# Optimization experiments

Hardware: AMD Instinct MI355X
Metric: run time of the kernel (lower is better)

## Reference

```python
import jax, jax.numpy as jnp
import numpy as np

B, S, DDENSE, D, V, F, K = 8192, 26, 13, 32, 100000, 8, 7


def setup_inputs() -> dict:
    key = jax.random.key(0)
    ks = jax.random.split(key, 24)
    n = lambda i, shape, s=0.05: (jax.random.normal(ks[i], shape, dtype=jnp.float32) * s)
    return {
        'sparse_inputs': jax.random.randint(ks[0], (B, S), 0, V),
        'dense_inputs': jax.random.normal(ks[1], (B, DDENSE), dtype=jnp.float32),
        'gen_table': n(2, (V, D), 0.1), 'gen_W': n(3, (DDENSE, D)), 'gen_b': jnp.zeros((D,), jnp.float32),
        'cls_table': n(4, (V, D), 0.1), 'cls_W': n(5, (DDENSE, D)), 'cls_b': jnp.zeros((D,), jnp.float32),
        'conv_k0': n(6, (K, 1, 1, F)), 'conv_b0': jnp.zeros((F,), jnp.float32),
        'fc_W0': n(7, (13 * D * F, 3 * D)), 'fc_b0': jnp.zeros((3 * D,), jnp.float32),
        'conv_k1': n(8, (K, 1, F, F)), 'conv_b1': jnp.zeros((F,), jnp.float32),
        'fc_W1': n(9, (6 * D * F, 3 * D)), 'fc_b1': jnp.zeros((3 * D,), jnp.float32),
        'mlp_W1': n(10, (1584, 128)), 'mlp_b1': jnp.zeros((128,), jnp.float32),
        'bn_gamma': jnp.ones((128,), jnp.float32), 'bn_beta': jnp.zeros((128,), jnp.float32),
        'bn_mean': jnp.zeros((128,), jnp.float32), 'bn_var': jnp.ones((128,), jnp.float32),
        'out_W': n(11, (128, 1)), 'out_b': jnp.zeros((1,), jnp.float32),
    }


def _embed(sparse_inputs, dense_inputs, table, W, b):
    sp = table[sparse_inputs]                       # [B, 26, 32]
    dn = (dense_inputs @ W + b)[:, None, :]         # [B, 1, 32]
    return jnp.concatenate([sp, dn], axis=1)        # [B, 27, 32]


def _conv_tanh(x, k, b):
    y = jax.lax.conv_general_dilated(x, k, (1, 1), 'SAME',
                                     dimension_numbers=('NHWC', 'HWIO', 'NHWC'))
    return jnp.tanh(y + b)


def _maxpool2(x):  # MaxPooling2D((2,1), padding='valid') on NHWC
    return jax.lax.reduce_window(x, -jnp.inf, jax.lax.max,
                                 (1, 2, 1, 1), (1, 2, 1, 1), 'VALID')


def _forward(sparse_inputs, dense_inputs, gen_table, gen_W, gen_b,
             cls_table, cls_W, cls_b, conv_k0, conv_b0, fc_W0, fc_b0,
             conv_k1, conv_b1, fc_W1, fc_b1, mlp_W1, mlp_b1,
             bn_gamma, bn_beta, bn_mean, bn_var, out_W, out_b):
    embs_gen = _embed(sparse_inputs, dense_inputs, gen_table, gen_W, gen_b)
    embs_cls = _embed(sparse_inputs, dense_inputs, cls_table, cls_W, cls_b)

    x = embs_gen[..., None]                         # [B, 27, 32, 1] NHWC
    new_feats = []
    for ck, cb, fw, fb in ((conv_k0, conv_b0, fc_W0, fc_b0),
                           (conv_k1, conv_b1, fc_W1, fc_b1)):
        x = _maxpool2(_conv_tanh(x, ck, cb))
        flat = x.reshape(x.shape[0], -1)
        new_feats.append(jnp.tanh(flat @ fw + fb))  # [B, 96]

    gen = jnp.concatenate(new_feats, axis=1).reshape(x.shape[0], -1, D)  # [B, 6, 32]
    aug = jnp.concatenate([embs_cls, gen], axis=1)                       # [B, 33, 32]

    # pairwise inner products = upper triangle of Gram matrix, combinations order
    gram = jnp.einsum('bnd,bmd->bnm', aug, aug)
    iu, ju = jnp.triu_indices(aug.shape[1], k=1)
    ip = gram[:, iu, ju]                            # [B, 528]

    h = jnp.concatenate([ip, aug.reshape(aug.shape[0], -1)], axis=1)     # [B, 1584]
    h = jax.nn.relu(h @ mlp_W1 + mlp_b1)
    h = (h - bn_mean) * jax.lax.rsqrt(bn_var + 1e-3) * bn_gamma + bn_beta
    return jax.nn.sigmoid(h @ out_W + out_b)        # [B, 1]


def reference(sparse_inputs, dense_inputs, gen_table, gen_W, gen_b,
              cls_table, cls_W, cls_b, conv_k0, conv_b0, fc_W0, fc_b0,
              conv_k1, conv_b1, fc_W1, fc_b1, mlp_W1, mlp_b1,
              bn_gamma, bn_beta, bn_mean, bn_var, out_W, out_b):
    return _forward(sparse_inputs, dense_inputs, gen_table, gen_W, gen_b,
                    cls_table, cls_W, cls_b, conv_k0, conv_b0, fc_W0, fc_b0,
                    conv_k1, conv_b1, fc_W1, fc_b1, mlp_W1, mlp_b1,
                    bn_gamma, bn_beta, bn_mean, bn_var, out_W, out_b)
```

## Files before the change

### kernel.cpp

```cpp
#include <hip/hip_runtime.h>
#include <hip/hip_bf16.h>
#include <math.h>

#define BATCH 8192

typedef unsigned short bf16_t;
typedef _Float16 f16_t;
typedef __attribute__((ext_vector_type(2))) _Float16 h2_t;
typedef __attribute__((ext_vector_type(8))) short short8;
typedef __attribute__((ext_vector_type(4))) float f32x4;

union U32H2 { unsigned int u; h2_t h; };

__device__ __forceinline__ float bf2f(bf16_t u) {
    union { unsigned int i; float f; } v; v.i = ((unsigned int)u) << 16; return v.f;
}
__device__ __forceinline__ bf16_t f2bf(float f) {
    union { float f; unsigned int i; } v; v.f = f;
    unsigned int x = v.i;
    unsigned int r = (x + 0x7FFFu + ((x >> 16) & 1u)) >> 16;
    return (bf16_t)r;
}
__device__ __forceinline__ float fast_tanh(float x) {
    float ax = fabsf(x);
    float e = __expf(ax + ax);
    float t = 1.0f - 2.0f * __builtin_amdgcn_rcpf(e + 1.0f);
    return copysignf(t, x);
}


__device__ __forceinline__ void wpack_one(
    const float* __restrict__ src, bf16_t* __restrict__ dst,
    int P, int N, int NT, int Ksrc)
{
    int e = P & 7, lane = (P >> 3) & 63, idx = P >> 9;
    int nt = idx % NT, git = idx / NT;
    int n = nt * 16 + (lane & 15);
    int k = git * 32 + (lane >> 4) * 8 + e;
    dst[P] = (k < Ksrc) ? f2bf(src[(size_t)k * N + n]) : (bf16_t)0;
}

__global__ __launch_bounds__(256) void k_wpack(
    const float* __restrict__ W0, const float* __restrict__ W1, const float* __restrict__ W2,
    bf16_t* __restrict__ Wt0, bf16_t* __restrict__ Wt1, bf16_t* __restrict__ Wt2)
{
    const int m = blockIdx.y;
    const int P = blockIdx.x * 256 + threadIdx.x;
    if (m == 0)      { if (P < 319488) wpack_one(W0, Wt0, P, 96, 6, 3328); }
    else if (m == 1) { if (P < 147456) wpack_one(W1, Wt1, P, 96, 6, 1536); }
    else             { if (P < 204800) wpack_one(W2, Wt2, P, 128, 8, 1584); }
}

__global__ __launch_bounds__(256) void k_conv_fused(
    const int* __restrict__ sp, const float* __restrict__ dn,
    const float* __restrict__ gen_table, const float* __restrict__ gen_W, const float* __restrict__ gen_b,
    const float* __restrict__ k0, const float* __restrict__ b0,
    const float* __restrict__ k1, const float* __restrict__ b1,
    bf16_t* __restrict__ pooled0, bf16_t* __restrict__ pooled1)
{
    __shared__ float embGt[2][32][28];
    __shared__ unsigned int x0[2 * 13 * 32 * 4];
    __shared__ float k0s[56], k1s[448], b0s[8], b1s[8];
    __shared__ int ids[52];
    __shared__ float dloc[26];
    const int t = threadIdx.x;
    const int half = t >> 7, tt = t & 127;
    const int b = blockIdx.x * 2 + half;

    if (tt < 26) ids[half * 26 + tt] = sp[b * 26 + tt];
    if (tt >= 32 && tt < 45) dloc[half * 13 + tt - 32] = dn[b * 13 + (tt - 32)];
    if (t < 56) k0s[t] = k0[t];
    if (t >= 64 && t < 72) b0s[t - 64] = b0[t - 64];
    if (t >= 72 && t < 80) b1s[t - 72] = b1[t - 72];
    for (int i = t; i < 448; i += 256) k1s[i] = k1[i];
    __syncthreads();

    for (int i = tt; i < 416; i += 128) {
        int s_ = i >> 4, d = (i & 15) * 2;
        float2 v = *(const float2*)(gen_table + (size_t)ids[half * 26 + s_] * 32 + d);
        embGt[half][d][s_] = v.x;
        embGt[half][d + 1][s_] = v.y;
    }
    if (tt < 32) {
        float a = gen_b[tt];
        #pragma unroll
        for (int k = 0; k < 13; k++) a += dloc[half * 13 + k] * gen_W[k * 32 + tt];
        embGt[half][tt][26] = a;
    }
    __syncthreads();

    bf16_t* p0base = pooled0 + ((size_t)(b >> 4) * 416) * 128 + (b & 15) * 8;

    {
        const int w = tt >> 2, f0 = (tt & 3) * 2;
        const float* xp = &embGt[half][w][0];
        float xr[28];
        #pragma unroll
        for (int q = 0; q < 7; q++) {
            float4 v = *(const float4*)(xp + 4 * q);
            xr[4 * q] = v.x; xr[4 * q + 1] = v.y; xr[4 * q + 2] = v.z; xr[4 * q + 3] = v.w;
        }
        float k0r[7][2];
        #pragma unroll
        for (int tap = 0; tap < 7; tap++) {
            k0r[tap][0] = k0s[tap * 8 + f0];
            k0r[tap][1] = k0s[tap * 8 + f0 + 1];
        }
        const float b00 = b0s[f0], b01 = b0s[f0 + 1];
        #pragma unroll
        for (int hp = 0; hp < 13; hp++) {
            float p00 = b00, p01 = b01, p10 = b00, p11 = b01;
            #pragma unroll
            for (int tap = 0; tap < 7; tap++) {
                const int h0 = 2 * hp + tap - 3;
                if (h0 >= 0 && h0 < 27) {
                    p00 += xr[h0] * k0r[tap][0];
                    p01 += xr[h0] * k0r[tap][1];
                }
                const int h1 = 2 * hp + 1 + tap - 3;
                if (h1 >= 0 && h1 < 27) {
                    p10 += xr[h1] * k0r[tap][0];
                    p11 += xr[h1] * k0r[tap][1];
                }
            }
            float m0 = fast_tanh(fmaxf(p00, p10));
            float m1 = fast_tanh(fmaxf(p01, p11));
            unsigned int pk = (unsigned int)f2bf(m0) | ((unsigned int)f2bf(m1) << 16);
            *(unsigned int*)(p0base + (hp * 32 + w) * 128 + f0) = pk;
            U32H2 hx; hx.h = h2_t{(f16_t)m0, (f16_t)m1};
            x0[half * 1664 + hp * 128 + w * 4 + (tt & 3)] = hx.u;
        }
    }
    __syncthreads();

    {
        const int w1 = t >> 3, fo = t & 7;
        h2_t kh[7][4];
        #pragma unroll
        for (int tap = 0; tap < 7; tap++)
            #pragma unroll
            for (int q = 0; q < 4; q++)
                kh[tap][q] = h2_t{(f16_t)k1s[tap * 64 + (2 * q) * 8 + fo],
                                  (f16_t)k1s[tap * 64 + (2 * q + 1) * 8 + fo]};
        const f16_t bbh = (f16_t)b1s[fo];

        #pragma unroll
        for (int s = 0; s < 2; s++) {
            h2_t acc[12];
            #pragma unroll
            for (int r = 0; r < 12; r++) acc[r] = h2_t{bbh, (f16_t)0.f};
            #pragma unroll
            for (int hh = 0; hh < 13; hh++) {
                uint4 v = *(const uint4*)&x0[s * 1664 + hh * 128 + w1 * 4];
                U32H2 c0, c1, c2, c3;
                c0.u = v.x; c1.u = v.y; c2.u = v.z; c3.u = v.w;
                h2_t x2[4] = { c0.h, c1.h, c2.h, c3.h };
                #pragma unroll
                for (int tap = 0; tap < 7; tap++) {
                    const int r = hh + 3 - tap;
                    if (r >= 0 && r < 12) {
                        #pragma unroll
                        for (int q = 0; q < 4; q++) acc[r] += x2[q] * kh[tap][q];
                    }
                }
            }
            const int bs = blockIdx.x * 2 + s;
            bf16_t* p1base = pooled1 + ((size_t)(bs >> 4) * 192) * 128 + (bs & 15) * 8;
            #pragma unroll
            for (int hp = 0; hp < 6; hp++) {
                float a0 = (float)acc[2 * hp][0] + (float)acc[2 * hp][1];
                float a1 = (float)acc[2 * hp + 1][0] + (float)acc[2 * hp + 1][1];
                float m = fast_tanh(fmaxf(a0, a1));
                p1base[(hp * 32 + w1) * 128 + fo] = f2bf(m);
            }
        }
    }
}

__global__ __launch_bounds__(256) void k_fc_mfma(
    const bf16_t* __restrict__ A0, const bf16_t* __restrict__ Wt0, float* __restrict__ P0,
    const bf16_t* __restrict__ A1, const bf16_t* __restrict__ Wt1, float* __restrict__ P1)
{
    const int which = blockIdx.z;
    const bf16_t* A  = which ? A1 : A0;
    const bf16_t* Wt = which ? Wt1 : Wt0;
    float* P = (which ? P1 : P0) + (size_t)blockIdx.y * (BATCH * 96);
    const int K = which ? 1536 : 3328;
    const int iters = which ? 12 : 26;

    const int t = threadIdx.x, w = t >> 6, l = t & 63;
    const int lane15 = l & 15, quad = l >> 4;
    const int rb = blockIdx.x * 4 + w;
    const int kb = blockIdx.y * (K >> 2);

    const bf16_t* ap = A + ((size_t)rb * (K >> 3) + (kb >> 3) + quad) * 128 + lane15 * 8;
    const bf16_t* bp = Wt + (size_t)(kb >> 5) * 3072 + l * 8;
    f32x4 acc[6] = {};

    #pragma unroll 2
    for (int it = 0; it < iters; it++) {
        short8 a = *(const short8*)(ap + it * 512);
        #pragma unroll
        for (int nt = 0; nt < 6; nt++) {
            short8 bf = *(const short8*)(bp + it * 3072 + nt * 512);
            acc[nt] = __builtin_amdgcn_mfma_f32_16x16x32_bf16(a, bf, acc[nt], 0, 0, 0);
        }
    }
    const int baser = blockIdx.x * 64 + w * 16 + quad * 4;
    #pragma unroll
    for (int nt = 0; nt < 6; nt++)
        #pragma unroll
        for (int i = 0; i < 4; i++)
            P[(size_t)(baser + i) * 96 + nt * 16 + lane15] = acc[nt][i];
}

__global__ __launch_bounds__(256) void k_build_h(
    const int* __restrict__ sp, const float* __restrict__ dn,
    const float* __restrict__ cls_table, const float* __restrict__ cls_W, const float* __restrict__ cls_b,
    const float* __restrict__ p0, const float* __restrict__ fb0,
    const float* __restrict__ p1, const float* __restrict__ fb1,
    bf16_t* __restrict__ h)
{
    __shared__ bf16_t augs[4][33][40];
    __shared__ float grams[4][32][34];
    const int t = threadIdx.x, wv = t >> 6, l = t & 63;
    const int b = blockIdx.x * 4 + wv;
    bf16_t (*aug)[40] = augs[wv];
    float (*gram)[34] = grams[wv];

    const int myid = (l < 26) ? sp[b * 26 + l] : 0;

    for (int i = l; i < 416; i += 64) {
        int s_ = i >> 4, d = (i & 15) * 2;
        int id = __shfl(myid, s_);
        float2 v = *(const float2*)(cls_table + (size_t)id * 32 + d);
        unsigned int pk = (unsigned int)f2bf(v.x) | ((unsigned int)f2bf(v.y) << 16);
        *(unsigned int*)&aug[s_][d] = pk;
    }
    if (l < 32) {
        float a = cls_b[l];
        #pragma unroll
        for (int k = 0; k < 13; k++) a += dn[b * 13 + k] * cls_W[k * 32 + l];
        aug[26][l] = f2bf(a);
    }
    for (int i = l; i < 192; i += 64) {
        int n = 27 + (i >> 5), d = i & 31;
        float s;
        if (i < 96) {
            size_t o = (size_t)b * 96 + i;
            s = p0[o] + p0[o + 786432] + p0[o + 2 * 786432] + p0[o + 3 * 786432] + fb0[i];
        } else {
            int j = i - 96; size_t o = (size_t)b * 96 + j;
            s = p1[o] + p1[o + 786432] + p1[o + 2 * 786432] + p1[o + 3 * 786432] + fb1[j];
        }
        aug[n][d] = f2bf(fast_tanh(s));
    }

    const int m16 = l & 15, quad = l >> 4;
    short8 a0 = *(const short8*)&aug[m16][quad * 8];
    short8 a1 = *(const short8*)&aug[16 + m16][quad * 8];
    f32x4 c00 = {}, c01 = {}, c11 = {};
    c00 = __builtin_amdgcn_mfma_f32_16x16x32_bf16(a0, a0, c00, 0, 0, 0);
    c01 = __builtin_amdgcn_mfma_f32_16x16x32_bf16(a0, a1, c01, 0, 0, 0);
    c11 = __builtin_amdgcn_mfma_f32_16x16x32_bf16(a1, a1, c11, 0, 0, 0);
    #pragma unroll
    for (int i = 0; i < 4; i++) {
        gram[quad * 4 + i][m16] = c00[i];
        gram[quad * 4 + i][16 + m16] = c01[i];
        gram[16 + quad * 4 + i][16 + m16] = c11[i];
    }
    if (l < 32) {
        float s = 0.f;
        #pragma unroll
        for (int kk = 0; kk < 16; kk++) {
            unsigned int x = *(const unsigned int*)&aug[l][2 * kk];
            unsigned int y = *(const unsigned int*)&aug[32][2 * kk];
            s += bf2f((bf16_t)(x & 0xFFFFu)) * bf2f((bf16_t)(y & 0xFFFFu));
            s += bf2f((bf16_t)(x >> 16)) * bf2f((bf16_t)(y >> 16));
        }
        gram[l][32] = s;
    }

    bf16_t* hbp = h + ((size_t)(b >> 4) * 200) * 128 + (b & 15) * 8;
    for (int idx = l; idx < 528; idx += 64) {
        int k = 528 + 2 * idx;
        *(unsigned int*)(hbp + (k >> 3) * 128 + (k & 7)) = *(const unsigned int*)&aug[idx >> 4][(idx & 15) * 2];
    }
    if (l < 8) {
        int k = 1584 + 2 * l;
        *(unsigned int*)(hbp + (k >> 3) * 128 + (k & 7)) = 0u;
    }
    for (int pp = l; pp < 264; pp += 64) {
        int p = 2 * pp;
        int i = (int)((65.0f - sqrtf(4225.0f - 8.0f * (float)p)) * 0.5f);
        int st = (i * (65 - i)) >> 1;
        if (st > p) { i--; st = (i * (65 - i)) >> 1; }
        else { int st2 = ((i + 1) * (64 - i)) >> 1; if (st2 <= p) { i++; st = st2; } }
        int j = i + 1 + (p - st);
        float s0, s1;
        if (j < 32) { s0 = gram[i][j]; s1 = gram[i][j + 1]; }
        else        { s0 = gram[i][32]; s1 = gram[i + 1][i + 2]; }
        unsigned int pk = (unsigned int)f2bf(s0) | ((unsigned int)f2bf(s1) << 16);
        *(unsigned int*)(hbp + (p >> 3) * 128 + (p & 7)) = pk;
    }
}

__global__ __launch_bounds__(256) void k_mlp_mfma(
    const bf16_t* __restrict__ h, const bf16_t* __restrict__ Wt2,
    const float* __restrict__ b1, const float* __restrict__ gamma,
    const float* __restrict__ beta, const float* __restrict__ mean,
    const float* __restrict__ var, const float* __restrict__ outW,
    const float* __restrict__ outb, float* __restrict__ out)
{
    __shared__ float lds[2 * 16 * 65];
    __shared__ float red2[32];
    const int t = threadIdx.x, w = t >> 6, l = t & 63;
    const int lane15 = l & 15, quad = l >> 4;
    const int nhalf = w & 1, khalf = w >> 1;

    const bf16_t* ap = h + ((size_t)blockIdx.x * 200 + khalf * 100 + quad) * 128 + lane15 * 8;
    const bf16_t* bp = Wt2 + ((size_t)khalf * 25 * 8 + nhalf * 4) * 512 + l * 8;
    f32x4 acc[4] = {};

    #pragma unroll 2
    for (int it = 0; it < 25; it++) {
        short8 a = *(const short8*)(ap + it * 512);
        #pragma unroll
        for (int nt = 0; nt < 4; nt++) {
            short8 bf = *(const short8*)(bp + it * 4096 + nt * 512);
            acc[nt] = __builtin_amdgcn_mfma_f32_16x16x32_bf16(a, bf, acc[nt], 0, 0, 0);
        }
    }

    if (khalf == 1) {
        #pragma unroll
        for (int nt = 0; nt < 4; nt++)
            #pragma unroll
            for (int i = 0; i < 4; i++)
                lds[nhalf * 1040 + (quad * 4 + i) * 65 + nt * 16 + lane15] = acc[nt][i];
    }
    __syncthreads();
    if (khalf == 0) {
        float pl[4] = { 0.f, 0.f, 0.f, 0.f };
        #pragma unroll
        for (int nt = 0; nt < 4; nt++) {
            int c = nhalf * 64 + nt * 16 + lane15;
            float sc = gamma[c] * rsqrtf(var[c] + 1e-3f);
            float sh = beta[c] - mean[c] * sc;
            float ow = outW[c], bb = b1[c];
            #pragma unroll
            for (int i = 0; i < 4; i++) {
                float v = acc[nt][i] + lds[nhalf * 1040 + (quad * 4 + i) * 65 + nt * 16 + lane15] + bb;
                v = fmaxf(v, 0.f);
                pl[i] += (v * sc + sh) * ow;
            }
        }
        #pragma unroll
        for (int m = 1; m < 16; m <<= 1)
            #pragma unroll
            for (int i = 0; i < 4; i++) pl[i] += __shfl_xor(pl[i], m);
        if (lane15 == 0) {
            #pragma unroll
            for (int i = 0; i < 4; i++) red2[(quad * 4 + i) * 2 + nhalf] = pl[i];
        }
    }
    __syncthreads();
    if (t < 16) {
        float s = red2[t * 2] + red2[t * 2 + 1] + outb[0];
        out[blockIdx.x * 16 + t] = 1.f / (1.f + __expf(-s));
    }
}

extern "C" void kernel_launch(void* const* d_in, const int* in_sizes, int n_in,
                              void* d_out, int out_size, void* d_ws, size_t ws_size,
                              hipStream_t stream) {
    const int*   sp       = (const int*)d_in[0];
    const float* dn       = (const float*)d_in[1];
    const float* gen_tab  = (const float*)d_in[2];
    const float* gen_W    = (const float*)d_in[3];
    const float* gen_b    = (const float*)d_in[4];
    const float* cls_tab  = (const float*)d_in[5];
    const float* cls_W    = (const float*)d_in[6];
    const float* cls_b    = (const float*)d_in[7];
    const float* conv_k0  = (const float*)d_in[8];
    const float* conv_b0  = (const float*)d_in[9];
    const float* fc_W0    = (const float*)d_in[10];
    const float* fc_b0    = (const float*)d_in[11];
    const float* conv_k1  = (const float*)d_in[12];
    const float* conv_b1  = (const float*)d_in[13];
    const float* fc_W1    = (const float*)d_in[14];
    const float* fc_b1    = (const float*)d_in[15];
    const float* mlp_W1   = (const float*)d_in[16];
    const float* mlp_b1   = (const float*)d_in[17];
    const float* bn_gamma = (const float*)d_in[18];
    const float* bn_beta  = (const float*)d_in[19];
    const float* bn_mean  = (const float*)d_in[20];
    const float* bn_var   = (const float*)d_in[21];
    const float* out_W    = (const float*)d_in[22];
    const float* out_b    = (const float*)d_in[23];
    float* out = (float*)d_out;

    char* ws = (char*)d_ws;
    bf16_t* pooled0 = (bf16_t*)(ws + 0);
    bf16_t* pooled1 = (bf16_t*)(ws + 54525952ULL);
    float*  p0      = (float*)(ws + 79691776ULL);
    float*  p1      = (float*)(ws + 92274688ULL);
    bf16_t* Wt0     = (bf16_t*)(ws + 104857600ULL);
    bf16_t* Wt1     = (bf16_t*)(ws + 105496576ULL);
    bf16_t* Wt2     = (bf16_t*)(ws + 105791488ULL);
    bf16_t* h       = (bf16_t*)(ws + 0);

    k_wpack<<<dim3(1248, 3), 256, 0, stream>>>(fc_W0, fc_W1, mlp_W1, Wt0, Wt1, Wt2);
    k_conv_fused<<<BATCH / 2, 256, 0, stream>>>(sp, dn, gen_tab, gen_W, gen_b,
                                                conv_k0, conv_b0, conv_k1, conv_b1,
                                                pooled0, pooled1);
    k_fc_mfma<<<dim3(BATCH / 64, 4, 2), 256, 0, stream>>>(pooled0, Wt0, p0, pooled1, Wt1, p1);
    k_build_h<<<BATCH / 4, 256, 0, stream>>>(sp, dn, cls_tab, cls_W, cls_b,
                                             p0, fc_b0, p1, fc_b1, h);
    k_mlp_mfma<<<BATCH / 16, 256, 0, stream>>>(h, Wt2, mlp_b1, bn_gamma, bn_beta,
                                               bn_mean, bn_var, out_W, out_b, out);
}
```

Before: 248.5 us.

## Vectorize pooled/h global stores via LDS staging and fp16 conv0

```diff
diff --git a/kernel.cpp b/kernel.cpp
--- a/kernel.cpp
+++ b/kernel.cpp
@@ -27,7 +27,12 @@
     float t = 1.0f - 2.0f * __builtin_amdgcn_rcpf(e + 1.0f);
     return copysignf(t, x);
 }
-
+__device__ __forceinline__ h2_t hmax2(h2_t a, h2_t b) {
+    h2_t r;
+    r[0] = a[0] > b[0] ? a[0] : b[0];
+    r[1] = a[1] > b[1] ? a[1] : b[1];
+    return r;
+}
 
 __device__ __forceinline__ void wpack_one(
     const float* __restrict__ src, bf16_t* __restrict__ dst,
@@ -60,6 +65,7 @@
 {
     __shared__ float embGt[2][32][28];
     __shared__ unsigned int x0[2 * 13 * 32 * 4];
+    __shared__ bf16_t stage1[2][192][8];
     __shared__ float k0s[56], k1s[448], b0s[8], b1s[8];
     __shared__ int ids[52];
     __shared__ float dloc[26];
@@ -89,46 +95,61 @@
     }
     __syncthreads();
 
-    bf16_t* p0base = pooled0 + ((size_t)(b >> 4) * 416) * 128 + (b & 15) * 8;
-
     {
-        const int w = tt >> 2, f0 = (tt & 3) * 2;
-        const float* xp = &embGt[half][w][0];
-        float xr[28];
-        #pragma unroll
-        for (int q = 0; q < 7; q++) {
-            float4 v = *(const float4*)(xp + 4 * q);
-            xr[4 * q] = v.x; xr[4 * q + 1] = v.y; xr[4 * q + 2] = v.z; xr[4 * q + 3] = v.w;
-        }
-        float k0r[7][2];
-        #pragma unroll
-        for (int tap = 0; tap < 7; tap++) {
-            k0r[tap][0] = k0s[tap * 8 + f0];
-            k0r[tap][1] = k0s[tap * 8 + f0 + 1];
-        }
-        const float b00 = b0s[f0], b01 = b0s[f0 + 1];
-        #pragma unroll
-        for (int hp = 0; hp < 13; hp++) {
-            float p00 = b00, p01 = b01, p10 = b00, p11 = b01;
-            #pragma unroll
-            for (int tap = 0; tap < 7; tap++) {
-                const int h0 = 2 * hp + tap - 3;
-                if (h0 >= 0 && h0 < 27) {
-                    p00 += xr[h0] * k0r[tap][0];
-                    p01 += xr[h0] * k0r[tap][1];
+        h2_t k0h[7][4], b0h[4];
+        #pragma unroll
+        for (int tap = 0; tap < 7; tap++)
+            #pragma unroll
+            for (int q = 0; q < 4; q++)
+                k0h[tap][q] = h2_t{(f16_t)k0s[tap * 8 + 2 * q], (f16_t)k0s[tap * 8 + 2 * q + 1]};
+        #pragma unroll
+        for (int q = 0; q < 4; q++)
+            b0h[q] = h2_t{(f16_t)b0s[2 * q], (f16_t)b0s[2 * q + 1]};
+
+        #pragma unroll
+        for (int pi = 0; pi < 4; pi++) {
+            int pos = t + pi * 256;
+            if (pos < 832) {
+                int s = (pos >= 416) ? 1 : 0;
+                int q_ = pos - s * 416;
+                int hp = q_ >> 5, w = q_ & 31;
+                int bb = blockIdx.x * 2 + s;
+                const float* xp = &embGt[s][w][0];
+                f16_t xs[8];
+                #pragma unroll
+                for (int j = 0; j < 8; j++) {
+                    int hh = 2 * hp - 3 + j;
+                    float v = (hh >= 0 && hh < 27) ? xp[hh] : 0.f;
+                    xs[j] = (f16_t)v;
                 }
-                const int h1 = 2 * hp + 1 + tap - 3;
-                if (h1 >= 0 && h1 < 27) {
-                    p10 += xr[h1] * k0r[tap][0];
-                    p11 += xr[h1] * k0r[tap][1];
+                h2_t acc0[4], acc1[4];
+                #pragma unroll
+                for (int q = 0; q < 4; q++) { acc0[q] = b0h[q]; acc1[q] = b0h[q]; }
+                #pragma unroll
+                for (int tap = 0; tap < 7; tap++) {
+                    h2_t s0 = h2_t{xs[tap], xs[tap]};
+                    h2_t s1 = h2_t{xs[tap + 1], xs[tap + 1]};
+                    #pragma unroll
+                    for (int q = 0; q < 4; q++) {
+                        acc0[q] += s0 * k0h[tap][q];
+                        acc1[q] += s1 * k0h[tap][q];
+                    }
                 }
+                unsigned int outw[4], xw[4];
+                #pragma unroll
+                for (int q = 0; q < 4; q++) {
+                    h2_t mx = hmax2(acc0[q], acc1[q]);
+                    float t0 = fast_tanh((float)mx[0]);
+                    float t1 = fast_tanh((float)mx[1]);
+                    outw[q] = (unsigned int)f2bf(t0) | ((unsigned int)f2bf(t1) << 16);
+                    U32H2 hx; hx.h = h2_t{(f16_t)t0, (f16_t)t1};
+                    xw[q] = hx.u;
+                }
+                uint4 ov = make_uint4(outw[0], outw[1], outw[2], outw[3]);
+                *(uint4*)(pooled0 + (((size_t)(bb >> 4) * 416 + hp * 32 + w) * 128 + (bb & 15) * 8)) = ov;
+                uint4 xv = make_uint4(xw[0], xw[1], xw[2], xw[3]);
+                *(uint4*)&x0[s * 1664 + hp * 128 + w * 4] = xv;
             }
-            float m0 = fast_tanh(fmaxf(p00, p10));
-            float m1 = fast_tanh(fmaxf(p01, p11));
-            unsigned int pk = (unsigned int)f2bf(m0) | ((unsigned int)f2bf(m1) << 16);
-            *(unsigned int*)(p0base + (hp * 32 + w) * 128 + f0) = pk;
-            U32H2 hx; hx.h = h2_t{(f16_t)m0, (f16_t)m1};
-            x0[half * 1664 + hp * 128 + w * 4 + (tt & 3)] = hx.u;
         }
     }
     __syncthreads();
@@ -164,15 +185,24 @@
                     }
                 }
             }
-            const int bs = blockIdx.x * 2 + s;
-            bf16_t* p1base = pooled1 + ((size_t)(bs >> 4) * 192) * 128 + (bs & 15) * 8;
             #pragma unroll
             for (int hp = 0; hp < 6; hp++) {
                 float a0 = (float)acc[2 * hp][0] + (float)acc[2 * hp][1];
                 float a1 = (float)acc[2 * hp + 1][0] + (float)acc[2 * hp + 1][1];
                 float m = fast_tanh(fmaxf(a0, a1));
-                p1base[(hp * 32 + w1) * 128 + fo] = f2bf(m);
+                stage1[s][hp * 32 + w1][fo] = f2bf(m);
             }
+        }
+    }
+    __syncthreads();
+    {
+        #pragma unroll
+        for (int i = t; i < 384; i += 256) {
+            int s = (i >= 192) ? 1 : 0;
+            int c = i - s * 192;
+            int bs = blockIdx.x * 2 + s;
+            uint4 v = *(const uint4*)&stage1[s][c][0];
+            *(uint4*)(pooled1 + (((size_t)(bs >> 4) * 192 + c) * 128 + (bs & 15) * 8)) = v;
         }
     }
 }
@@ -223,10 +253,12 @@
 {
     __shared__ bf16_t augs[4][33][40];
     __shared__ float grams[4][32][34];
+    __shared__ bf16_t hrows[4][1600];
     const int t = threadIdx.x, wv = t >> 6, l = t & 63;
     const int b = blockIdx.x * 4 + wv;
     bf16_t (*aug)[40] = augs[wv];
     float (*gram)[34] = grams[wv];
+    bf16_t* hrow = hrows[wv];
 
     const int myid = (l < 26) ? sp[b * 26 + l] : 0;
 
@@ -281,15 +313,9 @@
         gram[l][32] = s;
     }
 
-    bf16_t* hbp = h + ((size_t)(b >> 4) * 200) * 128 + (b & 15) * 8;
-    for (int idx = l; idx < 528; idx += 64) {
-        int k = 528 + 2 * idx;
-        *(unsigned int*)(hbp + (k >> 3) * 128 + (k & 7)) = *(const unsigned int*)&aug[idx >> 4][(idx & 15) * 2];
-    }
-    if (l < 8) {
-        int k = 1584 + 2 * l;
-        *(unsigned int*)(hbp + (k >> 3) * 128 + (k & 7)) = 0u;
-    }
+    for (int idx = l; idx < 528; idx += 64)
+        *(unsigned int*)&hrow[528 + 2 * idx] = *(const unsigned int*)&aug[idx >> 4][(idx & 15) * 2];
+    if (l < 8) *(unsigned int*)&hrow[1584 + 2 * l] = 0u;
     for (int pp = l; pp < 264; pp += 64) {
         int p = 2 * pp;
         int i = (int)((65.0f - sqrtf(4225.0f - 8.0f * (float)p)) * 0.5f);
@@ -300,8 +326,12 @@
         float s0, s1;
         if (j < 32) { s0 = gram[i][j]; s1 = gram[i][j + 1]; }
         else        { s0 = gram[i][32]; s1 = gram[i + 1][i + 2]; }
-        unsigned int pk = (unsigned int)f2bf(s0) | ((unsigned int)f2bf(s1) << 16);
-        *(unsigned int*)(hbp + (p >> 3) * 128 + (p & 7)) = pk;
+        *(unsigned int*)&hrow[p] = (unsigned int)f2bf(s0) | ((unsigned int)f2bf(s1) << 16);
+    }
+    bf16_t* hbp = h + ((size_t)(b >> 4) * 200) * 128 + (b & 15) * 8;
+    for (int c = l; c < 200; c += 64) {
+        uint4 v = *(const uint4*)&hrow[c * 8];
+        *(uint4*)(hbp + (size_t)c * 128) = v;
     }
 }
 
```

New measurement: 241.6 us. 2.8% less time.
